# Kernel tuning notes

Hardware: AMD Instinct MI355X
Metric: run time of the kernel (lower is better)

The kernel has to match this reference:

```python
import jax, jax.numpy as jnp
import numpy as np

N = 500_000
N_GROUPS = 50_000
D_IN = 64
D_OUT = 64
IN_MLP = D_IN * 3  # x, x - min, x - max (use_num=False)
NEG_SLOPE = 0.2


def setup_inputs() -> dict:
    key = jax.random.key(0)
    k_x, k_c, k_w1, k_w2 = jax.random.split(key, 4)
    x = jax.random.normal(k_x, (N, D_IN), dtype=jnp.float32)
    # CSR pointer: 0 = p0 <= p1 <= ... <= p_{n_groups} = N
    inner = jnp.sort(jax.random.randint(k_c, (N_GROUPS - 1,), 0, N))
    csr_idx = jnp.concatenate([jnp.zeros((1,), jnp.int64 if jax.config.jax_enable_x64 else jnp.int32),
                               inner.astype(jnp.int32),
                               jnp.full((1,), N, jnp.int32)]).astype(jnp.int32)
    # MLP([in_mlp, d_out, d_out], bias=False): two bias-free Linear layers,
    # each followed by LeakyReLU(0.2) (BatchNorm omitted / identity).
    w1 = jax.random.normal(k_w1, (IN_MLP, D_OUT), dtype=jnp.float32) / np.sqrt(IN_MLP)
    w2 = jax.random.normal(k_w2, (D_OUT, D_OUT), dtype=jnp.float32) / np.sqrt(D_OUT)
    return {"x": x, "csr_idx": csr_idx, "w1": w1, "w2": w2}


def _forward(x, csr_idx, w1, w2):
    n = x.shape[0]
    # element -> segment id (jit-safe equivalent of repeat_interleave on lengths)
    seg = jnp.searchsorted(csr_idx, jnp.arange(n, dtype=csr_idx.dtype), side='right') - 1  # [N]
    # segment min/max + gather-back
    seg_min = jax.ops.segment_min(x, seg, num_segments=N_GROUPS)  # [G, D]
    seg_max = jax.ops.segment_max(x, seg, num_segments=N_GROUPS)  # [G, D]
    x_map_min = x - seg_min[seg]
    x_map_max = x - seg_max[seg]
    h = jnp.concatenate([x, x_map_min, x_map_max], axis=1)  # [N, 3*D_IN]
    h = jax.nn.leaky_relu(h @ w1, NEG_SLOPE)
    h = jax.nn.leaky_relu(h @ w2, NEG_SLOPE)
    return h


def reference(x, csr_idx, w1, w2):
    return _forward(x, csr_idx, w1, w2)
```

## Files before the change

kernel.cpp:

```cpp
#include <hip/hip_runtime.h>
#include <math.h>

#define NROWS 500000
#define NGRP  50000
#define NEG   0.2f
#define GPB   16

typedef __attribute__((ext_vector_type(8))) short bf16x8;
typedef __attribute__((ext_vector_type(4))) float f32x4;
typedef unsigned int uint32;

__device__ __forceinline__ float leaky(float h) { return h >= 0.f ? h : NEG * h; }
__device__ __forceinline__ unsigned short f2bf(float v) {
    uint32 u = __float_as_uint(v);
    u += 0x7FFFu + ((u >> 16) & 1u);
    return (unsigned short)(u >> 16);
}

__global__ void k0_frag(const float* __restrict__ w1, const float* __restrict__ w2,
                        unsigned short* __restrict__ wsf, unsigned short* __restrict__ w2f) {
    int r = blockIdx.x * 256 + threadIdx.x;
    if (r >= 4096) return;
    int j = r & 7, q = (r >> 3) & 3, n = (r >> 5) & 63, ks = r >> 11;
    int k = ks * 32 + q * 8 + j;
    float ws = w1[k * 64 + n] + w1[4096 + k * 64 + n] + w1[8192 + k * 64 + n];
    wsf[r] = f2bf(ws);
    w2f[r] = f2bf(w2[k * 64 + n]);
}

__global__ __launch_bounds__(256, 6)
void fused(const float* __restrict__ x, const int* __restrict__ csr,
           const float* __restrict__ w1,
           const unsigned short* __restrict__ wsf,
           const unsigned short* __restrict__ w2f,
           float* __restrict__ out) {
    __shared__ short xb[64 * 72];
    __shared__ short y1s[64 * 72];
    __shared__ float biasL[GPB * 65];
    __shared__ __align__(16) int rowgrpL[64];
    __shared__ int csrl[GPB + 1];

    const int tid = threadIdx.x, w = tid >> 6, lane = tid & 63;
    const int q = lane >> 4, nl = lane & 15;
    const int jb = __builtin_amdgcn_readfirstlane(w * 16);
    const int n = jb + nl;

    const int g0 = blockIdx.x * GPB;
    const int ng = min(GPB, NGRP - g0);
    if (tid <= ng) csrl[tid] = csr[g0 + tid];
    __syncthreads();
    const int p0 = csrl[0], p1 = csrl[ng];

    float* mnF = (float*)y1s;
    for (int gl = w; gl < ng; gl += 4) {
        int q0 = csrl[gl], q1 = csrl[gl + 1], cnt = q1 - q0;
        if (cnt > 0) {
            const float* p = x + (size_t)q0 * 64 + lane;
            float mn = INFINITY, mx = -INFINITY;
            int i = 0;
            for (; i + 4 <= cnt; i += 4) {
                float a = p[0], b = p[64], c = p[128], d = p[192];
                p += 256;
                mn = fminf(mn, fminf(fminf(a, b), fminf(c, d)));
                mx = fmaxf(mx, fmaxf(fmaxf(a, b), fmaxf(c, d)));
            }
            for (; i < cnt; ++i) { float a = p[0]; p += 64; mn = fminf(mn, a); mx = fmaxf(mx, a); }
            mnF[gl * 130 + lane]      = mn;
            mnF[gl * 130 + 64 + lane] = mx;
        }
    }
    __syncthreads();

    {
        const int gidx = lane < GPB ? lane : 0;
        float acc[16];
#pragma unroll
        for (int j = 0; j < 16; ++j) acc[j] = 0.f;
#pragma unroll 2
        for (int k = 0; k < 128; ++k) {
            float m = mnF[gidx * 130 + k];
            const float* __restrict__ wr = w1 + (64 + k) * 64 + jb;
#pragma unroll
            for (int j = 0; j < 16; ++j) acc[j] = fmaf(m, wr[j], acc[j]);
        }
        if (lane < ng) {
#pragma unroll
            for (int j = 0; j < 16; ++j) biasL[lane * 65 + jb + j] = -acc[j];
        }
    }
    __syncthreads();

    const bf16x8* wsv = (const bf16x8*)wsf;
    const bf16x8* w2v = (const bf16x8*)w2f;
    bf16x8 B0 = wsv[n * 4 + q];
    bf16x8 B1 = wsv[(64 + n) * 4 + q];
    bf16x8 C0 = w2v[n * 4 + q];
    bf16x8 C1 = w2v[(64 + n) * 4 + q];

    const int nch = (p1 - p0 + 63) >> 6;
    for (int ch = 0; ch < nch; ++ch) {
        const int r0c  = p0 + (ch << 6);
        const int rows = min(64, p1 - r0c);
        const int availf = rows * 64;

        const float4* x4 = (const float4*)(x + (size_t)r0c * 64);
#pragma unroll
        for (int i = 0; i < 4; ++i) {
            int f = (i * 256 + tid) * 4;
            if (f < availf) {
                float4 v = x4[f >> 2];
                int r = f >> 6, c = f & 63;
                uint32 lo = (uint32)f2bf(v.x) | ((uint32)f2bf(v.y) << 16);
                uint32 hi = (uint32)f2bf(v.z) | ((uint32)f2bf(v.w) << 16);
                *(uint32*)(&xb[r * 72 + c])     = lo;
                *(uint32*)(&xb[r * 72 + c + 2]) = hi;
            }
        }
        if (tid < 64) {
            int rs = min(r0c + tid, p1 - 1);
            int lo = 0, hi = ng;
#pragma unroll
            for (int it = 0; it < 5; ++it) {
                int mid = (lo + hi) >> 1;
                bool c = csrl[mid] <= rs;
                lo = c ? mid : lo;
                hi = c ? hi : mid;
            }
            rowgrpL[tid] = lo;
        }
        __syncthreads();

        f32x4 h[4];
#pragma unroll
        for (int mt = 0; mt < 4; ++mt) {
            int rbase = mt * 16 + q * 4;
            int4 grp = *(const int4*)(&rowgrpL[rbase]);
            f32x4 acc;
            acc.x = biasL[grp.x * 65 + n];
            acc.y = biasL[grp.y * 65 + n];
            acc.z = biasL[grp.z * 65 + n];
            acc.w = biasL[grp.w * 65 + n];
            bf16x8 a0 = *(const bf16x8*)(&xb[(mt * 16 + nl) * 72 + q * 8]);
            bf16x8 a1 = *(const bf16x8*)(&xb[(mt * 16 + nl) * 72 + 32 + q * 8]);
            acc = __builtin_amdgcn_mfma_f32_16x16x32_bf16(a0, B0, acc, 0, 0, 0);
            acc = __builtin_amdgcn_mfma_f32_16x16x32_bf16(a1, B1, acc, 0, 0, 0);
            h[mt] = acc;
        }
#pragma unroll
        for (int mt = 0; mt < 4; ++mt) {
            int rbase = mt * 16 + q * 4;
#pragma unroll
            for (int r = 0; r < 4; ++r)
                y1s[(rbase + r) * 72 + n] = (short)f2bf(leaky(h[mt][r]));
        }
        __syncthreads();

#pragma unroll
        for (int mt = 0; mt < 4; ++mt) {
            f32x4 acc = {0.f, 0.f, 0.f, 0.f};
            bf16x8 a0 = *(const bf16x8*)(&y1s[(mt * 16 + nl) * 72 + q * 8]);
            bf16x8 a1 = *(const bf16x8*)(&y1s[(mt * 16 + nl) * 72 + 32 + q * 8]);
            acc = __builtin_amdgcn_mfma_f32_16x16x32_bf16(a0, C0, acc, 0, 0, 0);
            acc = __builtin_amdgcn_mfma_f32_16x16x32_bf16(a1, C1, acc, 0, 0, 0);
            int rbase = mt * 16 + q * 4;
#pragma unroll
            for (int r = 0; r < 4; ++r) {
                int rl = rbase + r;
                if (rl < rows)
                    out[(size_t)(r0c + rl) * 64 + n] = leaky(acc[r]);
            }
        }
    }
}

extern "C" void kernel_launch(void* const* d_in, const int* in_sizes, int n_in,
                              void* d_out, int out_size, void* d_ws, size_t ws_size,
                              hipStream_t stream) {
    const float* x   = (const float*)d_in[0];
    const int*   csr = (const int*)d_in[1];
    const float* w1  = (const float*)d_in[2];
    const float* w2  = (const float*)d_in[3];
    float* out = (float*)d_out;

    unsigned short* wsf = (unsigned short*)d_ws;
    unsigned short* w2f = wsf + 4096;

    k0_frag<<<16, 256, 0, stream>>>(w1, w2, wsf, w2f);
    const int grid = (NGRP + GPB - 1) / GPB;
    fused<<<grid, 256, 0, stream>>>(x, csr, w1, wsf, w2f, out);
}
```

Measured before the change: 295.6 us.

## Vectorize segment min/max, MFMA split-bf16 bias, prefetch x chunks, nontemporal stores

The segment min/max scan now reads float4 rows, with four row-subgroups per wave reduced by shuffles. The per-group bias GEMV is replaced by MFMA using a hi/lo bf16 split of the weights and activations to keep near-fp32 accuracy. The next 64-row chunk of x is prefetched into registers while the current chunk is computed, and outputs use nontemporal stores. These changes add register pressure and extra MFMA work for the bias in exchange for fewer scalar loads and better latency hiding.

```diff
diff --git a/kernel.cpp b/kernel.cpp
--- a/kernel.cpp
+++ b/kernel.cpp
@@ -16,33 +16,44 @@
     u += 0x7FFFu + ((u >> 16) & 1u);
     return (unsigned short)(u >> 16);
 }
+__device__ __forceinline__ float bf2f(unsigned short h) {
+    return __uint_as_float((uint32)h << 16);
+}
 
 __global__ void k0_frag(const float* __restrict__ w1, const float* __restrict__ w2,
-                        unsigned short* __restrict__ wsf, unsigned short* __restrict__ w2f) {
+                        unsigned short* __restrict__ wsf, unsigned short* __restrict__ w2f,
+                        unsigned short* __restrict__ wbh, unsigned short* __restrict__ wbl) {
     int r = blockIdx.x * 256 + threadIdx.x;
-    if (r >= 4096) return;
-    int j = r & 7, q = (r >> 3) & 3, n = (r >> 5) & 63, ks = r >> 11;
-    int k = ks * 32 + q * 8 + j;
-    float ws = w1[k * 64 + n] + w1[4096 + k * 64 + n] + w1[8192 + k * 64 + n];
-    wsf[r] = f2bf(ws);
-    w2f[r] = f2bf(w2[k * 64 + n]);
+    if (r >= 8192) return;
+    int j = r & 7, q = (r >> 3) & 3, n = (r >> 5) & 63;
+    int k = (r >> 11) * 32 + q * 8 + j;
+    if (r < 4096) {
+        float ws = w1[k * 64 + n] + w1[4096 + k * 64 + n] + w1[8192 + k * 64 + n];
+        wsf[r] = f2bf(ws);
+        w2f[r] = f2bf(w2[k * 64 + n]);
+    }
+    float v = w1[(64 + k) * 64 + n];
+    unsigned short h = f2bf(v);
+    wbh[r] = h;
+    wbl[r] = f2bf(v - bf2f(h));
 }
 
 __global__ __launch_bounds__(256, 6)
 void fused(const float* __restrict__ x, const int* __restrict__ csr,
-           const float* __restrict__ w1,
            const unsigned short* __restrict__ wsf,
            const unsigned short* __restrict__ w2f,
+           const unsigned short* __restrict__ wbh,
+           const unsigned short* __restrict__ wbl,
            float* __restrict__ out) {
-    __shared__ short xb[64 * 72];
-    __shared__ short y1s[64 * 72];
+    __shared__ __align__(16) short xb[64 * 72];
+    __shared__ __align__(16) short y1s[64 * 72];
     __shared__ float biasL[GPB * 65];
     __shared__ __align__(16) int rowgrpL[64];
     __shared__ int csrl[GPB + 1];
 
     const int tid = threadIdx.x, w = tid >> 6, lane = tid & 63;
     const int q = lane >> 4, nl = lane & 15;
-    const int jb = __builtin_amdgcn_readfirstlane(w * 16);
+    const int jb = w * 16;
     const int n = jb + nl;
 
     const int g0 = blockIdx.x * GPB;
@@ -52,43 +63,78 @@
     const int p0 = csrl[0], p1 = csrl[ng];
 
     float* mnF = (float*)y1s;
-    for (int gl = w; gl < ng; gl += 4) {
-        int q0 = csrl[gl], q1 = csrl[gl + 1], cnt = q1 - q0;
-        if (cnt > 0) {
-            const float* p = x + (size_t)q0 * 64 + lane;
-            float mn = INFINITY, mx = -INFINITY;
-            int i = 0;
-            for (; i + 4 <= cnt; i += 4) {
-                float a = p[0], b = p[64], c = p[128], d = p[192];
-                p += 256;
-                mn = fminf(mn, fminf(fminf(a, b), fminf(c, d)));
-                mx = fmaxf(mx, fmaxf(fmaxf(a, b), fmaxf(c, d)));
-            }
-            for (; i < cnt; ++i) { float a = p[0]; p += 64; mn = fminf(mn, a); mx = fmaxf(mx, a); }
-            mnF[gl * 130 + lane]      = mn;
-            mnF[gl * 130 + 64 + lane] = mx;
+    {
+        const int sub = q;
+        const float4* xr = (const float4*)x;
+        for (int gl = w; gl < ng; gl += 4) {
+            int q0 = csrl[gl], cnt = csrl[gl + 1] - q0;
+            if (cnt <= 0) continue;
+            float4 mn = { INFINITY, INFINITY, INFINITY, INFINITY };
+            float4 mx = { -INFINITY, -INFINITY, -INFINITY, -INFINITY };
+            for (int i = 0; i < cnt; i += 16) {
+                int ra = q0 + min(i + sub,      cnt - 1);
+                int rb = q0 + min(i + sub + 4,  cnt - 1);
+                int rc = q0 + min(i + sub + 8,  cnt - 1);
+                int rd = q0 + min(i + sub + 12, cnt - 1);
+                float4 a = xr[ra * 16 + nl], b = xr[rb * 16 + nl];
+                float4 c = xr[rc * 16 + nl], d = xr[rd * 16 + nl];
+                mn.x = fminf(mn.x, fminf(fminf(a.x, b.x), fminf(c.x, d.x)));
+                mn.y = fminf(mn.y, fminf(fminf(a.y, b.y), fminf(c.y, d.y)));
+                mn.z = fminf(mn.z, fminf(fminf(a.z, b.z), fminf(c.z, d.z)));
+                mn.w = fminf(mn.w, fminf(fminf(a.w, b.w), fminf(c.w, d.w)));
+                mx.x = fmaxf(mx.x, fmaxf(fmaxf(a.x, b.x), fmaxf(c.x, d.x)));
+                mx.y = fmaxf(mx.y, fmaxf(fmaxf(a.y, b.y), fmaxf(c.y, d.y)));
+                mx.z = fmaxf(mx.z, fmaxf(fmaxf(a.z, b.z), fmaxf(c.z, d.z)));
+                mx.w = fmaxf(mx.w, fmaxf(fmaxf(a.w, b.w), fmaxf(c.w, d.w)));
+            }
+#pragma unroll
+            for (int mk = 16; mk <= 32; mk <<= 1) {
+                mn.x = fminf(mn.x, __shfl_xor(mn.x, mk));
+                mn.y = fminf(mn.y, __shfl_xor(mn.y, mk));
+                mn.z = fminf(mn.z, __shfl_xor(mn.z, mk));
+                mn.w = fminf(mn.w, __shfl_xor(mn.w, mk));
+                mx.x = fmaxf(mx.x, __shfl_xor(mx.x, mk));
+                mx.y = fmaxf(mx.y, __shfl_xor(mx.y, mk));
+                mx.z = fmaxf(mx.z, __shfl_xor(mx.z, mk));
+                mx.w = fmaxf(mx.w, __shfl_xor(mx.w, mk));
+            }
+            if (sub == 0) {
+                *(float4*)&mnF[gl * 132 + nl * 4]      = mn;
+                *(float4*)&mnF[gl * 132 + 64 + nl * 4] = mx;
+            }
         }
     }
     __syncthreads();
 
     {
-        const int gidx = lane < GPB ? lane : 0;
-        float acc[16];
-#pragma unroll
-        for (int j = 0; j < 16; ++j) acc[j] = 0.f;
-#pragma unroll 2
-        for (int k = 0; k < 128; ++k) {
-            float m = mnF[gidx * 130 + k];
-            const float* __restrict__ wr = w1 + (64 + k) * 64 + jb;
-#pragma unroll
-            for (int j = 0; j < 16; ++j) acc[j] = fmaf(m, wr[j], acc[j]);
-        }
-        if (lane < ng) {
-#pragma unroll
-            for (int j = 0; j < 16; ++j) biasL[lane * 65 + jb + j] = -acc[j];
-        }
-    }
-    __syncthreads();
+        const bf16x8* bhv = (const bf16x8*)wbh;
+        const bf16x8* blv = (const bf16x8*)wbl;
+        f32x4 acc = { 0.f, 0.f, 0.f, 0.f };
+#pragma unroll
+        for (int ks = 0; ks < 4; ++ks) {
+            bf16x8 Bh = bhv[(ks * 64 + n) * 4 + q];
+            bf16x8 Bl = blv[(ks * 64 + n) * 4 + q];
+            const float* ap = &mnF[nl * 132 + ks * 32 + q * 8];
+            f32x4 v0 = *(const f32x4*)ap;
+            f32x4 v1 = *(const f32x4*)(ap + 4);
+            bf16x8 ah, al;
+#pragma unroll
+            for (int jj = 0; jj < 4; ++jj) {
+                unsigned short h0 = f2bf(v0[jj]);
+                unsigned short h1 = f2bf(v1[jj]);
+                ah[jj]     = (short)h0;
+                ah[4 + jj] = (short)h1;
+                al[jj]     = (short)f2bf(v0[jj] - bf2f(h0));
+                al[4 + jj] = (short)f2bf(v1[jj] - bf2f(h1));
+            }
+            acc = __builtin_amdgcn_mfma_f32_16x16x32_bf16(ah, Bh, acc, 0, 0, 0);
+            acc = __builtin_amdgcn_mfma_f32_16x16x32_bf16(al, Bh, acc, 0, 0, 0);
+            acc = __builtin_amdgcn_mfma_f32_16x16x32_bf16(ah, Bl, acc, 0, 0, 0);
+        }
+#pragma unroll
+        for (int r = 0; r < 4; ++r)
+            biasL[(q * 4 + r) * 65 + n] = -acc[r];
+    }
 
     const bf16x8* wsv = (const bf16x8*)wsf;
     const bf16x8* w2v = (const bf16x8*)w2f;
@@ -98,17 +144,28 @@
     bf16x8 C1 = w2v[(64 + n) * 4 + q];
 
     const int nch = (p1 - p0 + 63) >> 6;
+    float4 stg[4];
+    {
+        int availf = min(64, p1 - p0) * 64;
+        const float4* x4 = (const float4*)(x + (size_t)p0 * 64);
+#pragma unroll
+        for (int i = 0; i < 4; ++i) {
+            int f = (i * 256 + tid) * 4;
+            if (f < availf) stg[i] = x4[f >> 2];
+        }
+    }
+    __syncthreads();
+
     for (int ch = 0; ch < nch; ++ch) {
         const int r0c  = p0 + (ch << 6);
         const int rows = min(64, p1 - r0c);
         const int availf = rows * 64;
 
-        const float4* x4 = (const float4*)(x + (size_t)r0c * 64);
 #pragma unroll
         for (int i = 0; i < 4; ++i) {
             int f = (i * 256 + tid) * 4;
             if (f < availf) {
-                float4 v = x4[f >> 2];
+                float4 v = stg[i];
                 int r = f >> 6, c = f & 63;
                 uint32 lo = (uint32)f2bf(v.x) | ((uint32)f2bf(v.y) << 16);
                 uint32 hi = (uint32)f2bf(v.z) | ((uint32)f2bf(v.w) << 16);
@@ -122,13 +179,24 @@
 #pragma unroll
             for (int it = 0; it < 5; ++it) {
                 int mid = (lo + hi) >> 1;
-                bool c = csrl[mid] <= rs;
-                lo = c ? mid : lo;
-                hi = c ? hi : mid;
+                bool cb = csrl[mid] <= rs;
+                lo = cb ? mid : lo;
+                hi = cb ? hi : mid;
             }
             rowgrpL[tid] = lo;
         }
         __syncthreads();
+
+        if (ch + 1 < nch) {
+            int r0n = r0c + 64;
+            int availn = min(64, p1 - r0n) * 64;
+            const float4* x4 = (const float4*)(x + (size_t)r0n * 64);
+#pragma unroll
+            for (int i = 0; i < 4; ++i) {
+                int f = (i * 256 + tid) * 4;
+                if (f < availn) stg[i] = x4[f >> 2];
+            }
+        }
 
         f32x4 h[4];
 #pragma unroll
@@ -167,7 +235,8 @@
             for (int r = 0; r < 4; ++r) {
                 int rl = rbase + r;
                 if (rl < rows)
-                    out[(size_t)(r0c + rl) * 64 + n] = leaky(acc[r]);
+                    __builtin_nontemporal_store(leaky(acc[r]),
+                        &out[(size_t)(r0c + rl) * 64 + n]);
             }
         }
     }
@@ -184,8 +253,10 @@
 
     unsigned short* wsf = (unsigned short*)d_ws;
     unsigned short* w2f = wsf + 4096;
-
-    k0_frag<<<16, 256, 0, stream>>>(w1, w2, wsf, w2f);
+    unsigned short* wbh = wsf + 8192;
+    unsigned short* wbl = wsf + 16384;
+
+    k0_frag<<<32, 256, 0, stream>>>(w1, w2, wsf, w2f, wbh, wbl);
     const int grid = (NGRP + GPB - 1) / GPB;
-    fused<<<grid, 256, 0, stream>>>(x, csr, w1, wsf, w2f, out);
-}
+    fused<<<grid, 256, 0, stream>>>(x, csr, wsf, w2f, wbh, wbl, out);
+}
```

Result: faster. 263.0 us (-11.0%).
